# Kernel optimization log

Hardware: AMD Instinct MI355X
Metric: run time of the kernel (lower is better)

The kernel has to match this reference:

```python
import jax, jax.numpy as jnp
import numpy as np

N = 500_000      # evaluation points
M = 8            # Nmode
K = 4            # Clebsch branches
NPSI = 256       # psi grid points
X0 = 0.0
H = 1.0 / (NPSI - 1)


def _cubic_interp(f, x):
    """Cubic Hermite spline (C1, FD slopes) on a uniform psi grid, extrapolating.
    f: [NPSI, C] table, x: [N] query points -> [N, C]."""
    u = (x - X0) / H
    i = jnp.clip(jnp.floor(u).astype(jnp.int32), 0, NPSI - 2)
    s = (u - i.astype(x.dtype))[:, None]           # local coord, may be outside [0,1] (extrap)
    d = jnp.gradient(f, axis=0) / H                # FD derivatives [NPSI, C]
    f0, f1, d0, d1 = f[i], f[i + 1], d[i], d[i + 1]
    s2 = s * s
    s3 = s2 * s
    return ((2 * s3 - 3 * s2 + 1) * f0 + (s3 - 2 * s2 + s) * H * d0
            + (-2 * s3 + 3 * s2) * f1 + (s3 - s2) * H * d1)


def setup_inputs() -> dict:
    key = jax.random.key(0)
    ks = jax.random.split(key, 12)
    pg = jnp.linspace(0.0, 1.0, NPSI, dtype=jnp.float32)
    inp = {
        "t": jnp.float32(0.5),
        "psi": jax.random.uniform(ks[0], (N,), jnp.float32, 0.05, 0.95),
        "theta": jax.random.uniform(ks[1], (N,), jnp.float32, -jnp.pi, jnp.pi),
        "varphi": jax.random.uniform(ks[2], (N,), jnp.float32, 0.0, 2 * jnp.pi),
        # smooth Clebsch profiles on the psi grid (safety factor q and alpha offset)
        "q_vals": (1.0 + 2.5 * pg ** 2).astype(jnp.float32),
        "aoff_vals": (0.3 * jnp.sin(2 * jnp.pi * pg)).astype(jnp.float32),
        "theta0": jax.random.uniform(ks[3], (M,), jnp.float32, -jnp.pi, jnp.pi),
        "omega": jax.random.uniform(ks[4], (M,), jnp.float32, 0.5, 2.0),
        "psi0": jax.random.uniform(ks[5], (M,), jnp.float32, 0.2, 0.8),
        "psi_scale": jax.random.uniform(ks[6], (M,), jnp.float32, 0.05, 0.15),
        "alpha_scale": jax.random.uniform(ks[7], (M,), jnp.float32, 0.2, 0.6),
        "gh_coefs": 0.5 * jax.random.normal(ks[8], (M, 4, 6), jnp.float32),
        "n": jax.random.randint(ks[9], (M,), 1, 12, jnp.int32),
    }
    return inp


def reference(t, psi, theta, varphi, q_vals, aoff_vals, theta0, omega, psi0,
              psi_scale, alpha_scale, gh_coefs, n):
    # Clebsch mapping: alpha_k(psi, theta) = q(psi) * (theta + 2*pi*k) + alpha_off(psi)
    qa = _cubic_interp(jnp.stack([q_vals, aoff_vals], axis=-1), psi)  # [N,2]
    q, aoff = qa[:, 0], qa[:, 1]
    kk = 2 * jnp.pi * jnp.arange(K, dtype=psi.dtype)
    alpha = q[:, None] * (theta[:, None] + kk[None, :]) + aoff[:, None]    # [N,K]
    # alpha0(psi; mode) table built from the Clebsch profiles (mirrors __init__)
    alpha0_grid = q_vals[:, None] * theta0[None, :] + aoff_vals[:, None]   # [NPSI,M]
    alpha0 = _cubic_interp(alpha0_grid, psi)                               # [N,M]

    x = (psi[:, None] - psi0) / psi_scale                                  # [N,M]
    y = (alpha[:, None, :] - alpha0[:, :, None]) / alpha_scale[None, :, None]  # [N,M,K]
    g = jnp.exp(-0.5 * (x[:, :, None] ** 2 + y ** 2))                      # [N,M,K]

    c = gh_coefs  # [M,4,6]
    h10 = x[:, :, None, None]
    h01 = y[:, :, :, None]
    h20 = (4 * x ** 2 - 2)[:, :, None, None]
    h11 = (x[:, :, None] * y)[:, :, :, None]
    h02 = (4 * y ** 2 - 2)[:, :, :, None]
    p = (c[None, :, None, :, 0] + c[None, :, None, :, 1] * h10
         + c[None, :, None, :, 2] * h01 + c[None, :, None, :, 3] * h20
         + c[None, :, None, :, 4] * h11 + c[None, :, None, :, 5] * h02)    # [N,M,K,4]
    p = p * g[:, :, :, None]

    nf = n.astype(psi.dtype)
    # alpha - alpha0 == y * alpha_scale
    phase = omega[None, :, None] * t - nf[None, :, None] * (
        varphi[:, None, None] - y * alpha_scale[None, :, None])            # [N,M,K]
    cp, sp = jnp.cos(phase), jnp.sin(phase)
    phi = jnp.sum(p[..., 0] * cp - p[..., 1] * sp, axis=(1, 2))            # [N]
    apar = jnp.sum(p[..., 2] * cp - p[..., 3] * sp, axis=(1, 2))           # [N]
    return phi, apar
```

## Files before the change

kernel.cpp:

```cpp
#include <hip/hip_runtime.h>

#define NPSI 256
#define MM 8
#define KK 4

typedef float v2f __attribute__((ext_vector_type(2)));

#if __has_builtin(__builtin_amdgcn_exp2f)
#define EXP2F(x) __builtin_amdgcn_exp2f(x)
#else
#define EXP2F(x) exp2f(x)
#endif
#define SIN_REV(x) __builtin_amdgcn_sinf(x)
#define COS_REV(x) __builtin_amdgcn_cosf(x)

#define VFMA(a,b,c) __builtin_elementwise_fma((v2f)(a),(v2f)(b),(v2f)(c))

__device__ inline float cubic_q(const float* __restrict__ q_vals, float psi) {
    float u = psi * (float)(NPSI - 1);
    int   i = (int)floorf(u);
    i = min(max(i, 0), NPSI - 2);
    float s  = u - (float)i;
    float f0 = q_vals[i];
    float f1 = q_vals[i + 1];
    float d0 = (i == 0)        ? (f1 - f0) : 0.5f * (f1 - q_vals[i - 1]);
    float d1 = (i == NPSI - 2) ? (f1 - f0) : 0.5f * (q_vals[i + 2] - f0);
    float s2 = s * s, s3 = s2 * s;
    return (2.f * s3 - 3.f * s2 + 1.f) * f0
         + (s3 - 2.f * s2 + s)         * d0
         + (-2.f * s3 + 3.f * s2)      * f1
         + (s3 - s2)                   * d1;
}

__global__ __launch_bounds__(256) void eik_kernel(
    const float* __restrict__ t_ptr,
    const float* __restrict__ psi_a,
    const float* __restrict__ theta_a,
    const float* __restrict__ varphi_a,
    const float* __restrict__ q_vals,
    const float* __restrict__ theta0_a,
    const float* __restrict__ omega_a,
    const float* __restrict__ psi0_a,
    const float* __restrict__ psi_scale_a,
    const float* __restrict__ alpha_scale_a,
    const float* __restrict__ gh_a,
    const int*   __restrict__ n_a,
    float* __restrict__ out,
    int N)
{
    const int gid   = blockIdx.x * blockDim.x + threadIdx.x;
    const int i0    = 2 * gid;
    if (i0 >= N) return;
    const bool full = (i0 + 1 < N);

    const float INV2PI = 0.15915494309189533577f;
    const float TWO_PI = 6.28318530717958647692f;
    const float NEXPC  = -0.72134752044448170368f;

    const float t = t_ptr[0];

    v2f psi, theta, varphi;
    if (full) {
        psi    = ((const v2f*)psi_a)[gid];
        theta  = ((const v2f*)theta_a)[gid];
        varphi = ((const v2f*)varphi_a)[gid];
    } else {
        psi.x = psi.y = psi_a[i0];
        theta.x = theta.y = theta_a[i0];
        varphi.x = varphi.y = varphi_a[i0];
    }

    v2f q;
    q.x = cubic_q(q_vals, psi.x);
    q.y = cubic_q(q_vals, psi.y);

    const v2f q2pi = q * TWO_PI;
    const float tt = t * INV2PI;
    const v2f  v2p = varphi * INV2PI;

    v2f phi = (v2f)0.f, apar = (v2f)0.f;

    #pragma unroll 1
    for (int m = 0; m < MM; ++m) {
        const float theta0 = theta0_a[m];
        const float omega  = omega_a[m];
        const float psi0   = psi0_a[m];
        const float inv_ps = __builtin_amdgcn_rcpf(psi_scale_a[m]);
        const float inv_as = __builtin_amdgcn_rcpf(alpha_scale_a[m]);
        const float nf     = (float)n_a[m];
        const float* c     = gh_a + m * 24;

        const v2f x  = (psi - psi0) * inv_ps;
        const v2f x2 = x * x;
        const v2f x4 = 4.f * x2;

        v2f pa[4], pb[4];
        float pf[4];
        #pragma unroll
        for (int comp = 0; comp < 4; ++comp) {
            const float c0 = c[comp*6+0], c1 = c[comp*6+1], c2 = c[comp*6+2];
            const float c3 = c[comp*6+3], c4 = c[comp*6+4], c5 = c[comp*6+5];
            const float a0 = fmaf(-2.f, c3 + c5, c0);
            pa[comp] = VFMA((v2f)c3, x4, VFMA((v2f)c1, x, (v2f)a0));
            pb[comp] = VFMA((v2f)c4, x, (v2f)c2);
            pf[comp] = c5;
        }

        const v2f dth  = theta - theta0;
        const v2f qdth = q * dth;
        v2f y          = qdth * inv_as;
        const v2f dy   = q2pi * inv_as;
        const v2f dphr = nf * q;
        const v2f p0r  = VFMA((v2f)nf, qdth * INV2PI,
                              VFMA((v2f)omega, (v2f)tt, -nf * v2p));

        v2f cp, sp, cd, sd;
        cp.x = COS_REV(p0r.x);  cp.y = COS_REV(p0r.y);
        sp.x = SIN_REV(p0r.x);  sp.y = SIN_REV(p0r.y);
        cd.x = COS_REV(dphr.x); cd.y = COS_REV(dphr.y);
        sd.x = SIN_REV(dphr.x); sd.y = SIN_REV(dphr.y);

        #pragma unroll
        for (int k = 0; k < KK; ++k) {
            const v2f t2 = VFMA(y, y, x2);
            const v2f y4 = VFMA((v2f)4.f, t2, -x4);
            const v2f ta = t2 * NEXPC;
            v2f g;
            g.x = EXP2F(ta.x);
            g.y = EXP2F(ta.y);
            const v2f gc = g * cp;
            const v2f gs = g * sp;
            const v2f p0 = VFMA((v2f)pf[0], y4, VFMA(pb[0], y, pa[0]));
            const v2f p1 = VFMA((v2f)pf[1], y4, VFMA(pb[1], y, pa[1]));
            const v2f p2 = VFMA((v2f)pf[2], y4, VFMA(pb[2], y, pa[2]));
            const v2f p3 = VFMA((v2f)pf[3], y4, VFMA(pb[3], y, pa[3]));
            phi  = VFMA(p0, gc, phi);
            phi  = VFMA(-p1, gs, phi);
            apar = VFMA(p2, gc, apar);
            apar = VFMA(-p3, gs, apar);
            if (k < KK - 1) {
                const v2f ncp = VFMA(cp, cd, -(sp * sd));
                const v2f nsp = VFMA(sp, cd,  cp * sd);
                cp = ncp; sp = nsp;
                y = y + dy;
            }
        }
    }

    if (full) {
        *(v2f*)(out + i0)     = phi;
        *(v2f*)(out + N + i0) = apar;
    } else {
        out[i0]     = phi.x;
        out[N + i0] = apar.x;
    }
}

extern "C" void kernel_launch(void* const* d_in, const int* in_sizes, int n_in,
                              void* d_out, int out_size, void* d_ws, size_t ws_size,
                              hipStream_t stream) {
    const float* t       = (const float*)d_in[0];
    const float* psi     = (const float*)d_in[1];
    const float* theta   = (const float*)d_in[2];
    const float* varphi  = (const float*)d_in[3];
    const float* q_vals  = (const float*)d_in[4];
    const float* theta0  = (const float*)d_in[6];
    const float* omega   = (const float*)d_in[7];
    const float* psi0    = (const float*)d_in[8];
    const float* psc     = (const float*)d_in[9];
    const float* asc     = (const float*)d_in[10];
    const float* gh      = (const float*)d_in[11];
    const int*   n_arr   = (const int*)d_in[12];

    const int N = in_sizes[1];
    float* out = (float*)d_out;

    const int npair = (N + 1) / 2;
    const int block = 256;
    const int grid  = (npair + block - 1) / block;
    eik_kernel<<<grid, block, 0, stream>>>(t, psi, theta, varphi, q_vals,
                                           theta0, omega, psi0, psc, asc,
                                           gh, n_arr, out, N);
}
```

Measured before the change: 94.87 us.

## Pack mode pairs into packed-float lanes instead of point pairs per thread

Each thread now handles one evaluation point and packs two modes into the v2f lanes, rather than two points per thread with one mode per iteration. The cubic q interpolation now runs once per thread, and there are twice as many threads, so the latency-bound work is spread more widely. The per-mode coefficient setup now loads two modes per iteration as vector pairs. Launch bounds request 8 blocks per unit for occupancy. The cost is that per-mode setup is repeated per point, and the coefficient loads are scattered scalar loads that get packed.

Result: slower. 97.26 us (+2.5%).

```diff
diff --git a/kernel.cpp b/kernel.cpp
--- a/kernel.cpp
+++ b/kernel.cpp
@@ -32,7 +32,7 @@
          + (s3 - s2)                   * d1;
 }
 
-__global__ __launch_bounds__(256) void eik_kernel(
+__global__ __launch_bounds__(256, 8) void eik_kernel(
     const float* __restrict__ t_ptr,
     const float* __restrict__ psi_a,
     const float* __restrict__ theta_a,
@@ -48,71 +48,68 @@
     float* __restrict__ out,
     int N)
 {
-    const int gid   = blockIdx.x * blockDim.x + threadIdx.x;
-    const int i0    = 2 * gid;
-    if (i0 >= N) return;
-    const bool full = (i0 + 1 < N);
+    const int gid = blockIdx.x * blockDim.x + threadIdx.x;
+    if (gid >= N) return;
 
     const float INV2PI = 0.15915494309189533577f;
     const float TWO_PI = 6.28318530717958647692f;
     const float NEXPC  = -0.72134752044448170368f;
 
-    const float t = t_ptr[0];
+    const float t     = t_ptr[0];
+    const float psi   = psi_a[gid];
+    const float theta = theta_a[gid];
+    const float vp    = varphi_a[gid] * INV2PI;
 
-    v2f psi, theta, varphi;
-    if (full) {
-        psi    = ((const v2f*)psi_a)[gid];
-        theta  = ((const v2f*)theta_a)[gid];
-        varphi = ((const v2f*)varphi_a)[gid];
-    } else {
-        psi.x = psi.y = psi_a[i0];
-        theta.x = theta.y = theta_a[i0];
-        varphi.x = varphi.y = varphi_a[i0];
-    }
-
-    v2f q;
-    q.x = cubic_q(q_vals, psi.x);
-    q.y = cubic_q(q_vals, psi.y);
-
-    const v2f q2pi = q * TWO_PI;
-    const float tt = t * INV2PI;
-    const v2f  v2p = varphi * INV2PI;
+    const float q    = cubic_q(q_vals, psi);
+    const float q2pi = q * TWO_PI;
+    const float tt   = t * INV2PI;
 
     v2f phi = (v2f)0.f, apar = (v2f)0.f;
 
     #pragma unroll 1
-    for (int m = 0; m < MM; ++m) {
-        const float theta0 = theta0_a[m];
-        const float omega  = omega_a[m];
-        const float psi0   = psi0_a[m];
-        const float inv_ps = __builtin_amdgcn_rcpf(psi_scale_a[m]);
-        const float inv_as = __builtin_amdgcn_rcpf(alpha_scale_a[m]);
-        const float nf     = (float)n_a[m];
-        const float* c     = gh_a + m * 24;
+    for (int mp = 0; mp < MM / 2; ++mp) {
+        const int m = 2 * mp;
+        const v2f theta0 = *(const v2f*)(theta0_a + m);
+        const v2f omega  = *(const v2f*)(omega_a + m);
+        const v2f psi0   = *(const v2f*)(psi0_a + m);
+        const v2f psc    = *(const v2f*)(psi_scale_a + m);
+        const v2f asc    = *(const v2f*)(alpha_scale_a + m);
+        v2f inv_ps, inv_as, nf;
+        inv_ps.x = __builtin_amdgcn_rcpf(psc.x);
+        inv_ps.y = __builtin_amdgcn_rcpf(psc.y);
+        inv_as.x = __builtin_amdgcn_rcpf(asc.x);
+        inv_as.y = __builtin_amdgcn_rcpf(asc.y);
+        nf.x = (float)n_a[m];
+        nf.y = (float)n_a[m + 1];
+        const float* cA = gh_a + m * 24;
+        const float* cB = gh_a + (m + 1) * 24;
 
-        const v2f x  = (psi - psi0) * inv_ps;
+        const v2f x  = ((v2f)psi - psi0) * inv_ps;
         const v2f x2 = x * x;
         const v2f x4 = 4.f * x2;
 
-        v2f pa[4], pb[4];
-        float pf[4];
+        v2f pa[4], pb[4], pf[4];
         #pragma unroll
         for (int comp = 0; comp < 4; ++comp) {
-            const float c0 = c[comp*6+0], c1 = c[comp*6+1], c2 = c[comp*6+2];
-            const float c3 = c[comp*6+3], c4 = c[comp*6+4], c5 = c[comp*6+5];
-            const float a0 = fmaf(-2.f, c3 + c5, c0);
-            pa[comp] = VFMA((v2f)c3, x4, VFMA((v2f)c1, x, (v2f)a0));
-            pb[comp] = VFMA((v2f)c4, x, (v2f)c2);
+            const v2f c0 = { cA[comp*6+0], cB[comp*6+0] };
+            const v2f c1 = { cA[comp*6+1], cB[comp*6+1] };
+            const v2f c2 = { cA[comp*6+2], cB[comp*6+2] };
+            const v2f c3 = { cA[comp*6+3], cB[comp*6+3] };
+            const v2f c4 = { cA[comp*6+4], cB[comp*6+4] };
+            const v2f c5 = { cA[comp*6+5], cB[comp*6+5] };
+            const v2f a0 = VFMA((v2f)(-2.f), c3 + c5, c0);
+            pa[comp] = VFMA(c3, x4, VFMA(c1, x, a0));
+            pb[comp] = VFMA(c4, x, c2);
             pf[comp] = c5;
         }
 
-        const v2f dth  = theta - theta0;
+        const v2f dth  = (v2f)theta - theta0;
         const v2f qdth = q * dth;
         v2f y          = qdth * inv_as;
         const v2f dy   = q2pi * inv_as;
         const v2f dphr = nf * q;
-        const v2f p0r  = VFMA((v2f)nf, qdth * INV2PI,
-                              VFMA((v2f)omega, (v2f)tt, -nf * v2p));
+        const v2f p0r  = VFMA(nf, qdth * INV2PI,
+                              VFMA(omega, (v2f)tt, -nf * vp));
 
         v2f cp, sp, cd, sd;
         cp.x = COS_REV(p0r.x);  cp.y = COS_REV(p0r.y);
@@ -130,10 +127,10 @@
             g.y = EXP2F(ta.y);
             const v2f gc = g * cp;
             const v2f gs = g * sp;
-            const v2f p0 = VFMA((v2f)pf[0], y4, VFMA(pb[0], y, pa[0]));
-            const v2f p1 = VFMA((v2f)pf[1], y4, VFMA(pb[1], y, pa[1]));
-            const v2f p2 = VFMA((v2f)pf[2], y4, VFMA(pb[2], y, pa[2]));
-            const v2f p3 = VFMA((v2f)pf[3], y4, VFMA(pb[3], y, pa[3]));
+            const v2f p0 = VFMA(pf[0], y4, VFMA(pb[0], y, pa[0]));
+            const v2f p1 = VFMA(pf[1], y4, VFMA(pb[1], y, pa[1]));
+            const v2f p2 = VFMA(pf[2], y4, VFMA(pb[2], y, pa[2]));
+            const v2f p3 = VFMA(pf[3], y4, VFMA(pb[3], y, pa[3]));
             phi  = VFMA(p0, gc, phi);
             phi  = VFMA(-p1, gs, phi);
             apar = VFMA(p2, gc, apar);
@@ -147,13 +144,8 @@
         }
     }
 
-    if (full) {
-        *(v2f*)(out + i0)     = phi;
-        *(v2f*)(out + N + i0) = apar;
-    } else {
-        out[i0]     = phi.x;
-        out[N + i0] = apar.x;
-    }
+    out[gid]     = phi.x + phi.y;
+    out[N + gid] = apar.x + apar.y;
 }
 
 extern "C" void kernel_launch(void* const* d_in, const int* in_sizes, int n_in,
@@ -175,9 +167,8 @@
     const int N = in_sizes[1];
     float* out = (float*)d_out;
 
-    const int npair = (N + 1) / 2;
     const int block = 256;
-    const int grid  = (npair + block - 1) / block;
+    const int grid  = (N + block - 1) / block;
     eik_kernel<<<grid, block, 0, stream>>>(t, psi, theta, varphi, q_vals,
                                            theta0, omega, psi0, psc, asc,
                                            gh, n_arr, out, N);
```
